# Optimization experiments

Hardware: AMD Instinct MI355X
Metric: run time of the kernel (lower is better)

The kernel has to match this reference:

```python
import jax, jax.numpy as jnp
import numpy as np

IN_DIM = 128
OUT_DIM = 128
H = 8
HD = OUT_DIM // H  # 16
EPS = 1e-5
NEG = -1e30


def setup_inputs() -> dict:
    key = jax.random.key(0)
    ks = jax.random.split(key, 10)
    B, N = 8, 1024
    h = jax.random.normal(ks[0], (B, N, IN_DIM), dtype=jnp.float32)
    adj_mask = jax.random.randint(ks[1], (B, N, N), 0, 2, dtype=jnp.int32)
    s = 1.0 / np.sqrt(IN_DIM)
    W = jax.random.normal(ks[2], (H, IN_DIM, HD), dtype=jnp.float32) * s
    a = jax.random.normal(ks[3], (H, 2 * HD), dtype=jnp.float32) * (1.0 / np.sqrt(2 * HD))
    ln1_g = jnp.ones((OUT_DIM,), jnp.float32)
    ln1_b = jnp.zeros((OUT_DIM,), jnp.float32)
    w1 = jax.random.normal(ks[4], (OUT_DIM, 2 * OUT_DIM), dtype=jnp.float32) * (1.0 / np.sqrt(OUT_DIM))
    b1 = jnp.zeros((2 * OUT_DIM,), jnp.float32)
    w2 = jax.random.normal(ks[5], (2 * OUT_DIM, OUT_DIM), dtype=jnp.float32) * (1.0 / np.sqrt(2 * OUT_DIM))
    b2 = jnp.zeros((OUT_DIM,), jnp.float32)
    ln2_g = jnp.ones((OUT_DIM,), jnp.float32)
    ln2_b = jnp.zeros((OUT_DIM,), jnp.float32)
    return dict(h=h, adj_mask=adj_mask, W=W, a=a, ln1_g=ln1_g, ln1_b=ln1_b,
                w1=w1, b1=b1, w2=w2, b2=b2, ln2_g=ln2_g, ln2_b=ln2_b)


def _layernorm(x, g, b):
    mu = jnp.mean(x, axis=-1, keepdims=True)
    var = jnp.mean(jnp.square(x - mu), axis=-1, keepdims=True)
    return (x - mu) * jax.lax.rsqrt(var + EPS) * g + b


def reference(h, adj_mask, W, a, ln1_g, ln1_b, w1, b1, w2, b2, ln2_g, ln2_b):
    B, N, _ = h.shape
    # Per-head projection: (B,H,N,HD)
    Wh = jnp.einsum('bni,hid->bhnd', h, W)
    # a.[Wh_i, Wh_j] = a_src.Wh_i + a_dst.Wh_j (decompose concat-score)
    a_src, a_dst = a[:, :HD], a[:, HD:]
    s_i = jnp.einsum('bhnd,hd->bhn', Wh, a_src)  # source term
    s_j = jnp.einsum('bhnd,hd->bhn', Wh, a_dst)  # target term
    e = s_i[:, :, :, None] + s_j[:, :, None, :]  # (B,H,N,N)
    e = jnp.where(e >= 0, e, 0.2 * e)            # LeakyReLU(0.2)
    mask = (adj_mask != 0)[:, None, :, :]        # (B,1,N,N)
    e = jnp.where(mask, e, NEG)
    alpha = jax.nn.softmax(e, axis=-1)
    # rows with no neighbors -> NaN in torch softmax -> zeroed; replicate
    row_valid = jnp.any(mask, axis=-1, keepdims=True)  # (B,1,N,1)
    alpha = jnp.where(row_valid, alpha, 0.0)
    # dropout in eval mode = identity
    h_heads = jnp.einsum('bhnm,bhmd->bhnd', alpha, Wh)
    h_cat = h_heads.transpose(0, 2, 1, 3).reshape(B, N, H * HD)
    # residual (in_dim == out_dim here)
    h_cat = _layernorm(h_cat + h, ln1_g, ln1_b)
    ffn = jnp.maximum(h_cat @ w1 + b1, 0.0) @ w2 + b2
    return _layernorm(h_cat + ffn, ln2_g, ln2_b)
```

## Files before the change

### kernel.cpp

```cpp
#include <hip/hip_runtime.h>
#include <hip/hip_bf16.h>

#define IN_DIM 128
#define OUT_DIM 128
#define NHEAD 8
#define HD 16
#define BB 8
#define NN 1024

typedef unsigned long long u64;
typedef float f32x4 __attribute__((ext_vector_type(4)));
typedef short bf16x8 __attribute__((ext_vector_type(8)));

__global__ __launch_bounds__(256) void k_pack(const int* __restrict__ adj,
                                              u64* __restrict__ bits) {
    int lane = threadIdx.x & 63;
    int wid = blockIdx.x * 4 + (threadIdx.x >> 6);
    for (int w = wid; w < BB * NN * 16; w += 2048 * 4) {
        int v = adj[(size_t)w * 64 + lane];
        u64 m = __ballot(v != 0);
        if (lane == 0) bits[w] = m;
    }
}

__global__ __launch_bounds__(256) void k_wprep(const float* __restrict__ w1,
                                               const float* __restrict__ w2,
                                               unsigned short* __restrict__ w1T,
                                               unsigned short* __restrict__ w2T) {
    __shared__ float tile[32][33];
    int blk = blockIdx.x;
    const float* src; unsigned short* dst; int R, C;
    if (blk < 32) { src = w1; dst = w1T; R = 128; C = 256; }
    else          { src = w2; dst = w2T; R = 256; C = 128; blk -= 32; }
    int tpr = C >> 5;
    int tr = blk / tpr, tc = blk - tr * tpr;
    int r0 = tr << 5, c0 = tc << 5;
    int t = threadIdx.x, lr = t >> 5, lc = t & 31;
#pragma unroll
    for (int p = 0; p < 4; ++p)
        tile[lr + p * 8][lc] = src[(size_t)(r0 + lr + p * 8) * C + c0 + lc];
    __syncthreads();
#pragma unroll
    for (int p = 0; p < 4; ++p) {
        __hip_bfloat16 bv = __float2bfloat16(tile[lc][lr + p * 8]);
        dst[(size_t)(c0 + lr + p * 8) * R + r0 + lc] = *(unsigned short*)&bv;
    }
}

__global__ __launch_bounds__(256) void k_wh(const float* __restrict__ hin,
                                            const float* __restrict__ W,
                                            float* __restrict__ wh) {
    extern __shared__ float smem[];
    float* h_s  = smem;
    float* wt_s = smem + 32 * 132;
    int t = threadIdx.x;
    int blk = blockIdx.x;
    int b = blk >> 5;
    int ntile = blk & 31;
    const float* hrow = hin + ((size_t)b * NN + ntile * 32) * IN_DIM;

#pragma unroll
    for (int it = 0; it < 4; ++it) {
        int g = t + 256 * it;
        int row = g >> 5, c4 = g & 31;
        float4 v = ((const float4*)hrow)[g];
        *(float4*)&h_s[row * 132 + c4 * 4] = v;
    }
    for (int g = t; g < (NHEAD * IN_DIM * HD) / 4; g += 256) {
        int hh = g >> 9;
        int rem = g & 511;
        int i = rem >> 2, d4 = rem & 3;
        float4 v = ((const float4*)W)[g];
        wt_s[(hh * 16 + d4 * 4 + 0) * 132 + i] = v.x;
        wt_s[(hh * 16 + d4 * 4 + 1) * 132 + i] = v.y;
        wt_s[(hh * 16 + d4 * 4 + 2) * 132 + i] = v.z;
        wt_s[(hh * 16 + d4 * 4 + 3) * 132 + i] = v.w;
    }
    __syncthreads();

    int hq = (t & 31) >> 2;
    int d4 = t & 3;
    int ngrp = t >> 5;
    float acc[4][4];
#pragma unroll
    for (int q = 0; q < 4; ++q)
#pragma unroll
        for (int dd = 0; dd < 4; ++dd) acc[q][dd] = 0.f;

    for (int i4 = 0; i4 < 32; ++i4) {
        float4 wr[4], hv[4];
#pragma unroll
        for (int dd = 0; dd < 4; ++dd)
            wr[dd] = *(const float4*)&wt_s[(hq * 16 + d4 * 4 + dd) * 132 + i4 * 4];
#pragma unroll
        for (int q = 0; q < 4; ++q)
            hv[q] = *(const float4*)&h_s[(ngrp * 4 + q) * 132 + i4 * 4];
#pragma unroll
        for (int q = 0; q < 4; ++q)
#pragma unroll
            for (int dd = 0; dd < 4; ++dd)
                acc[q][dd] += hv[q].x * wr[dd].x + hv[q].y * wr[dd].y +
                              hv[q].z * wr[dd].z + hv[q].w * wr[dd].w;
    }
#pragma unroll
    for (int q = 0; q < 4; ++q) {
        int row = ntile * 32 + ngrp * 4 + q;
        float4 o = make_float4(acc[q][0], acc[q][1], acc[q][2], acc[q][3]);
        *(float4*)&wh[(((size_t)b * NHEAD + hq) * NN + row) * HD + d4 * 4] = o;
    }
}

__global__ __launch_bounds__(512) void k_attn(const float* __restrict__ wh,
                                              const unsigned* __restrict__ bits32,
                                              const float* __restrict__ a,
                                              float* __restrict__ hh) {
    __shared__ __align__(16) float a_s[32];
    __shared__ unsigned mask_s[128 * 33];
    __shared__ __align__(16) float sj_s[NN];
    __shared__ float si_s[128];
    __shared__ __align__(16) unsigned short whT[16 * 1032];

    int t = threadIdx.x;
    int blk = blockIdx.x;
    int part = blk & 7;
    int bh = blk >> 3;
    int hq = bh & 7;
    int b = bh >> 3;
    int blkrow = part * 128;
    const float* whg = wh + (size_t)bh * (NN * HD);

    if (t < 32) a_s[t] = a[hq * 32 + t];

    {
        const unsigned* mb = bits32 + ((size_t)b * NN + blkrow) * 32;
#pragma unroll
        for (int it = 0; it < 8; ++it) {
            int g = t + 512 * it;
            int row = g >> 5, w = g & 31;
            mask_s[row * 33 + w] = mb[g];
        }
    }
    {
        int d = t & 15, jg = t >> 4;
        const float* src = whg + d;
#pragma unroll
        for (int jj = 0; jj < 32; jj += 2) {
            int j = jg * 32 + jj;
            float v0 = src[(size_t)j * 16];
            float v1 = src[(size_t)(j + 1) * 16];
            unsigned u;
            asm("v_cvt_pk_bf16_f32 %0, %1, %2" : "=v"(u) : "v"(v0), "v"(v1));
            *(unsigned*)&whT[d * 1032 + j] = u;
        }
    }
    __syncthreads();

    {
        float4 ad0 = *(const float4*)&a_s[16];
        float4 ad1 = *(const float4*)&a_s[20];
        float4 ad2 = *(const float4*)&a_s[24];
        float4 ad3 = *(const float4*)&a_s[28];
#pragma unroll
        for (int r = 0; r < 2; ++r) {
            int j = t * 2 + r;
            const float4* p = (const float4*)(whg + (size_t)j * 16);
            float4 x0 = p[0], x1 = p[1], x2 = p[2], x3 = p[3];
            sj_s[j] = x0.x * ad0.x + x0.y * ad0.y + x0.z * ad0.z + x0.w * ad0.w +
                      x1.x * ad1.x + x1.y * ad1.y + x1.z * ad1.z + x1.w * ad1.w +
                      x2.x * ad2.x + x2.y * ad2.y + x2.z * ad2.z + x2.w * ad2.w +
                      x3.x * ad3.x + x3.y * ad3.y + x3.z * ad3.z + x3.w * ad3.w;
        }
        if (t < 128) {
            float4 as0 = *(const float4*)&a_s[0];
            float4 as1 = *(const float4*)&a_s[4];
            float4 as2 = *(const float4*)&a_s[8];
            float4 as3 = *(const float4*)&a_s[12];
            int i = blkrow + t;
            const float4* p = (const float4*)(whg + (size_t)i * 16);
            float4 x0 = p[0], x1 = p[1], x2 = p[2], x3 = p[3];
            si_s[t] = x0.x * as0.x + x0.y * as0.y + x0.z * as0.z + x0.w * as0.w +
                      x1.x * as1.x + x1.y * as1.y + x1.z * as1.z + x1.w * as1.w +
                      x2.x * as2.x + x2.y * as2.y + x2.z * as2.z + x2.w * as2.w +
                      x3.x * as3.x + x3.y * as3.y + x3.z * as3.z + x3.w * as3.w;
        }
    }
    __syncthreads();

    int wv = t >> 6, lane = t & 63;
    int lo16 = lane & 15;
    int g = lane >> 4;
    float si_r = si_s[wv * 16 + lo16];
    const unsigned* mrow = &mask_s[(wv * 16 + lo16) * 33];

    f32x4 acc = {0.f, 0.f, 0.f, 0.f};
    float lsum = 0.f;

    for (int kt = 0; kt < 32; ++kt) {
        bf16x8 bfrag = *(const bf16x8*)&whT[lo16 * 1032 + kt * 32 + g * 8];
        float4 sa = *(const float4*)&sj_s[kt * 32 + g * 8];
        float4 sb = *(const float4*)&sj_s[kt * 32 + g * 8 + 4];
        unsigned m = mrow[kt] >> (g * 8);
        float p[8];
        float sj[8] = {sa.x, sa.y, sa.z, sa.w, sb.x, sb.y, sb.z, sb.w};
#pragma unroll
        for (int e = 0; e < 8; ++e) {
            float v = si_r + sj[e];
            v = fmaxf(v, 0.f) + 0.2f * fminf(v, 0.f);
            float pe = __expf(v);
            pe = ((m >> e) & 1) ? pe : 0.f;
            lsum += pe;
            p[e] = pe;
        }
        union { bf16x8 v; unsigned u[4]; } af;
#pragma unroll
        for (int q = 0; q < 4; ++q)
            asm("v_cvt_pk_bf16_f32 %0, %1, %2" : "=v"(af.u[q]) : "v"(p[2 * q]), "v"(p[2 * q + 1]));
        acc = __builtin_amdgcn_mfma_f32_16x16x32_bf16(af.v, bfrag, acc, 0, 0, 0);
    }

    lsum += __shfl_xor(lsum, 16);
    lsum += __shfl_xor(lsum, 32);

    float* obase = hh + ((size_t)b * NN + blkrow + wv * 16) * OUT_DIM + hq * HD + lo16;
#pragma unroll
    for (int q = 0; q < 4; ++q) {
        float ls = __shfl(lsum, 4 * g + q);
        float r = (ls > 0.f) ? 1.0f / ls : 0.f;
        obase[(size_t)(4 * g + q) * OUT_DIM] = acc[q] * r;
    }
}

__global__ __launch_bounds__(512, 1) void k_ffn(const float* __restrict__ hhs,
                                                const float* __restrict__ hin,
                                                const float* __restrict__ g1,
                                                const float* __restrict__ bt1,
                                                const unsigned short* __restrict__ w1T,
                                                const float* __restrict__ bb1,
                                                const unsigned short* __restrict__ w2T,
                                                const float* __restrict__ bb2,
                                                const float* __restrict__ g2,
                                                const float* __restrict__ bt2,
                                                float* __restrict__ out) {
    __shared__ float xc_f[32][128];
    __shared__ float y_f[32][132];
    __shared__ __align__(16) unsigned short xc_bf[32 * 128];
    __shared__ __align__(16) unsigned short hid_bf[32 * 256];

    int t = threadIdx.x;
    int R0 = blockIdx.x * 32;
    int wv = t >> 6, lane = t & 63;
    int lo = lane & 15, g = lane >> 4;

    bf16x8 b1f[2][4];
#pragma unroll
    for (int jt = 0; jt < 2; ++jt) {
        int n = (wv * 2 + jt) * 16 + lo;
#pragma unroll
        for (int kt = 0; kt < 4; ++kt)
            b1f[jt][kt] = *(const bf16x8*)&w1T[(size_t)n * 128 + kt * 32 + g * 8];
    }
    bf16x8 b2f[8];
    {
        int n = wv * 16 + lo;
#pragma unroll
        for (int kt = 0; kt < 8; ++kt)
            b2f[kt] = *(const bf16x8*)&w2T[(size_t)n * 256 + kt * 32 + g * 8];
    }
    float b1v[2];
    b1v[0] = bb1[(wv * 2 + 0) * 16 + lo];
    b1v[1] = bb1[(wv * 2 + 1) * 16 + lo];
    float b2v = bb2[wv * 16 + lo];

    {
        int r = t >> 4, c = t & 15;
        size_t row = (size_t)(R0 + r) * 128;
        float4 ha = *(const float4*)&hhs[row + c * 8];
        float4 hb = *(const float4*)&hhs[row + c * 8 + 4];
        float4 ia = *(const float4*)&hin[row + c * 8];
        float4 ib = *(const float4*)&hin[row + c * 8 + 4];
        float x[8] = {ha.x + ia.x, ha.y + ia.y, ha.z + ia.z, ha.w + ia.w,
                      hb.x + ib.x, hb.y + ib.y, hb.z + ib.z, hb.w + ib.w};
        float s = 0.f, s2 = 0.f;
#pragma unroll
        for (int j = 0; j < 8; ++j) { s += x[j]; s2 += x[j] * x[j]; }
#pragma unroll
        for (int off = 8; off > 0; off >>= 1) {
            s += __shfl_xor(s, off);
            s2 += __shfl_xor(s2, off);
        }
        float mu = s * (1.f / 128.f);
        float var = s2 * (1.f / 128.f) - mu * mu;
        float rs = rsqrtf(var + 1e-5f);
        float4 ga = *(const float4*)&g1[c * 8], gb = *(const float4*)&g1[c * 8 + 4];
        float4 ba = *(const float4*)&bt1[c * 8], bb = *(const float4*)&bt1[c * 8 + 4];
        float gg[8] = {ga.x, ga.y, ga.z, ga.w, gb.x, gb.y, gb.z, gb.w};
        float bbv[8] = {ba.x, ba.y, ba.z, ba.w, bb.x, bb.y, bb.z, bb.w};
        float xo[8];
#pragma unroll
        for (int j = 0; j < 8; ++j) xo[j] = (x[j] - mu) * rs * gg[j] + bbv[j];
        *(float4*)&xc_f[r][c * 8]     = make_float4(xo[0], xo[1], xo[2], xo[3]);
        *(float4*)&xc_f[r][c * 8 + 4] = make_float4(xo[4], xo[5], xo[6], xo[7]);
        union { uint4 v; unsigned u[4]; } pk;
#pragma unroll
        for (int q = 0; q < 4; ++q)
            asm("v_cvt_pk_bf16_f32 %0, %1, %2" : "=v"(pk.u[q]) : "v"(xo[2 * q]), "v"(xo[2 * q + 1]));
        int byte = (r * 256 + c * 16) ^ ((r & 7) << 4);
        *(uint4*)((char*)xc_bf + byte) = pk.v;
    }
    __syncthreads();

    {
        bf16x8 af[2][4];
#pragma unroll
        for (int mt = 0; mt < 2; ++mt) {
            int m = mt * 16 + lo;
#pragma unroll
            for (int kt = 0; kt < 4; ++kt) {
                int byte = (m * 256 + kt * 64 + g * 16) ^ ((m & 7) << 4);
                af[mt][kt] = *(const bf16x8*)((const char*)xc_bf + byte);
            }
        }
#pragma unroll
        for (int mt = 0; mt < 2; ++mt)
#pragma unroll
            for (int jt = 0; jt < 2; ++jt) {
                f32x4 acc = {0.f, 0.f, 0.f, 0.f};
#pragma unroll
                for (int kt = 0; kt < 4; ++kt)
                    acc = __builtin_amdgcn_mfma_f32_16x16x32_bf16(af[mt][kt], b1f[jt][kt], acc, 0, 0, 0);
                int n = (wv * 2 + jt) * 16 + lo;
#pragma unroll
                for (int q = 0; q < 4; ++q) {
                    float hv = fmaxf(acc[q] + b1v[jt], 0.f);
                    int m = mt * 16 + 4 * g + q;
                    int byte = (m * 512 + n * 2) ^ ((m & 7) << 4);
                    __hip_bfloat16 bv = __float2bfloat16(hv);
                    *(unsigned short*)((char*)hid_bf + byte) = *(unsigned short*)&bv;
                }
            }
    }
    __syncthreads();

    {
        f32x4 acc2[2] = {{0.f, 0.f, 0.f, 0.f}, {0.f, 0.f, 0.f, 0.f}};
#pragma unroll
        for (int mt = 0; mt < 2; ++mt) {
            int m = mt * 16 + lo;
#pragma unroll
            for (int kt = 0; kt < 8; ++kt) {
                int byte = (m * 512 + kt * 64 + g * 16) ^ ((m & 7) << 4);
                bf16x8 a = *(const bf16x8*)((const char*)hid_bf + byte);
                acc2[mt] = __builtin_amdgcn_mfma_f32_16x16x32_bf16(a, b2f[kt], acc2[mt], 0, 0, 0);
            }
        }
        int n = wv * 16 + lo;
#pragma unroll
        for (int mt = 0; mt < 2; ++mt)
#pragma unroll
            for (int q = 0; q < 4; ++q)
                y_f[mt * 16 + 4 * g + q][n] = acc2[mt][q] + b2v;
    }
    __syncthreads();

    {
        int r = t >> 4, c = t & 15;
        float xv[8];
        float s = 0.f, s2 = 0.f;
#pragma unroll
        for (int j = 0; j < 8; ++j) {
            float v = xc_f[r][c * 8 + j] + y_f[r][c * 8 + j];
            xv[j] = v; s += v; s2 += v * v;
        }
#pragma unroll
        for (int off = 8; off > 0; off >>= 1) {
            s += __shfl_xor(s, off);
            s2 += __shfl_xor(s2, off);
        }
        float mu = s * (1.f / 128.f);
        float var = s2 * (1.f / 128.f) - mu * mu;
        float rs = rsqrtf(var + 1e-5f);
        float4 ga = *(const float4*)&g2[c * 8], gb = *(const float4*)&g2[c * 8 + 4];
        float4 ba = *(const float4*)&bt2[c * 8], bb = *(const float4*)&bt2[c * 8 + 4];
        float o[8] = {(xv[0] - mu) * rs * ga.x + ba.x, (xv[1] - mu) * rs * ga.y + ba.y,
                      (xv[2] - mu) * rs * ga.z + ba.z, (xv[3] - mu) * rs * ga.w + ba.w,
                      (xv[4] - mu) * rs * gb.x + bb.x, (xv[5] - mu) * rs * gb.y + bb.y,
                      (xv[6] - mu) * rs * gb.z + bb.z, (xv[7] - mu) * rs * gb.w + bb.w};
        size_t row = (size_t)(R0 + r) * 128;
        *(float4*)&out[row + c * 8]     = make_float4(o[0], o[1], o[2], o[3]);
        *(float4*)&out[row + c * 8 + 4] = make_float4(o[4], o[5], o[6], o[7]);
    }
}

extern "C" void kernel_launch(void* const* d_in, const int* in_sizes, int n_in,
                              void* d_out, int out_size, void* d_ws, size_t ws_size,
                              hipStream_t stream) {
    const float* hin  = (const float*)d_in[0];
    const int*   adj  = (const int*)d_in[1];
    const float* W    = (const float*)d_in[2];
    const float* a    = (const float*)d_in[3];
    const float* ln1g = (const float*)d_in[4];
    const float* ln1b = (const float*)d_in[5];
    const float* w1   = (const float*)d_in[6];
    const float* b1   = (const float*)d_in[7];
    const float* w2   = (const float*)d_in[8];
    const float* b2   = (const float*)d_in[9];
    const float* ln2g = (const float*)d_in[10];
    const float* ln2b = (const float*)d_in[11];
    float* out = (float*)d_out;

    float* wh             = (float*)d_ws;
    u64*   bits           = (u64*)((char*)d_ws + (4u << 20));
    float* hh             = (float*)((char*)d_ws + (5u << 20));
    unsigned short* w1T   = (unsigned short*)((char*)d_ws + (9u << 20));
    unsigned short* w2T   = (unsigned short*)((char*)d_ws + (9u << 20) + 65536);

    k_pack<<<2048, 256, 0, stream>>>(adj, bits);
    k_wprep<<<64, 256, 0, stream>>>(w1, w2, w1T, w2T);
    k_wh<<<BB * 32, 256, (32 * 132 + 128 * 132) * sizeof(float), stream>>>(hin, W, wh);
    k_attn<<<BB * NHEAD * 8, 512, 0, stream>>>(wh, (const unsigned*)bits, a, hh);
    k_ffn<<<BB * NN / 32, 512, 0, stream>>>(hh, hin, ln1g, ln1b, w1T, b1, w2T, b2, ln2g, ln2b, out);
}
```

Baseline: 66.72 us.

## Merge prep kernels and precompute bf16 Wh and attention scores for attention

Folds the adjacency bit-packing, weight transpose and Wh projection into one prep kernel. The projection now emits bf16 transposed Wh plus per-node source and target scores pre-scaled by log2e, so the attention kernel no longer converts or recomputes them. The attention kernel loads bf16 Wh into an XOR-swizzled LDS layout, reads mask words straight from global with one-ahead prefetch, and computes LeakyReLU as fma(0.4,|v|,0.6v). It uses raw v_exp_f32 with -150 for masked entries and sets launch bounds to 3 blocks per CU. This cuts launches, LDS footprint and redundant setup, but reads W from global in the projection and makes mask loads uncoalesced.

```diff
diff --git a/kernel.cpp b/kernel.cpp
--- a/kernel.cpp
+++ b/kernel.cpp
@@ -7,207 +7,174 @@
 #define HD 16
 #define BB 8
 #define NN 1024
+#define LOG2E 1.44269504f
 
 typedef unsigned long long u64;
 typedef float f32x4 __attribute__((ext_vector_type(4)));
 typedef short bf16x8 __attribute__((ext_vector_type(8)));
 
-__global__ __launch_bounds__(256) void k_pack(const int* __restrict__ adj,
-                                              u64* __restrict__ bits) {
-    int lane = threadIdx.x & 63;
-    int wid = blockIdx.x * 4 + (threadIdx.x >> 6);
-    for (int w = wid; w < BB * NN * 16; w += 2048 * 4) {
-        int v = adj[(size_t)w * 64 + lane];
-        u64 m = __ballot(v != 0);
-        if (lane == 0) bits[w] = m;
+__global__ __launch_bounds__(256) void k_prep(
+    const float* __restrict__ hin, const float* __restrict__ W,
+    const float* __restrict__ a, const int* __restrict__ adj,
+    u64* __restrict__ bits, unsigned short* __restrict__ whT,
+    float* __restrict__ si_g, float* __restrict__ sj_g,
+    const float* __restrict__ w1, const float* __restrict__ w2,
+    unsigned short* __restrict__ w1T, unsigned short* __restrict__ w2T)
+{
+    __shared__ float smem[32 * 132];
+    int blk = blockIdx.x;
+    int t = threadIdx.x;
+
+    if (blk < 256) {
+        int b = blk >> 5, ntile = blk & 31;
+        const float* hrow = hin + ((size_t)b * NN + ntile * 32) * IN_DIM;
+#pragma unroll
+        for (int it = 0; it < 4; ++it) {
+            int g = t + 256 * it;
+            int row = g >> 5, c4 = g & 31;
+            float4 v = ((const float4*)hrow)[g];
+            *(float4*)&smem[row * 132 + c4 * 4] = v;
+        }
+        __syncthreads();
+
+        int d4 = t & 3;
+        int hq = (t >> 2) & 7;
+        int ngrp = t >> 5;
+        float acc[4][4];
+#pragma unroll
+        for (int q = 0; q < 4; ++q)
+#pragma unroll
+            for (int dd = 0; dd < 4; ++dd) acc[q][dd] = 0.f;
+
+        for (int i4 = 0; i4 < 32; ++i4) {
+            float4 wf[4];
+#pragma unroll
+            for (int k = 0; k < 4; ++k)
+                wf[k] = *(const float4*)&W[((size_t)hq * 128 + i4 * 4 + k) * 16 + d4 * 4];
+            float4 hv[4];
+#pragma unroll
+            for (int q = 0; q < 4; ++q)
+                hv[q] = *(const float4*)&smem[(ngrp * 4 + q) * 132 + i4 * 4];
+#pragma unroll
+            for (int q = 0; q < 4; ++q) {
+                acc[q][0] += hv[q].x * wf[0].x + hv[q].y * wf[1].x + hv[q].z * wf[2].x + hv[q].w * wf[3].x;
+                acc[q][1] += hv[q].x * wf[0].y + hv[q].y * wf[1].y + hv[q].z * wf[2].y + hv[q].w * wf[3].y;
+                acc[q][2] += hv[q].x * wf[0].z + hv[q].y * wf[1].z + hv[q].z * wf[2].z + hv[q].w * wf[3].z;
+                acc[q][3] += hv[q].x * wf[0].w + hv[q].y * wf[1].w + hv[q].z * wf[2].w + hv[q].w * wf[3].w;
+            }
+        }
+
+        int bh = b * NHEAD + hq;
+        int rowbase = ntile * 32 + ngrp * 4;
+
+        float asrc[4], adst[4];
+#pragma unroll
+        for (int dd = 0; dd < 4; ++dd) {
+            asrc[dd] = a[hq * 32 + d4 * 4 + dd];
+            adst[dd] = a[hq * 32 + 16 + d4 * 4 + dd];
+        }
+#pragma unroll
+        for (int q = 0; q < 4; ++q) {
+            float psi = acc[q][0] * asrc[0] + acc[q][1] * asrc[1] + acc[q][2] * asrc[2] + acc[q][3] * asrc[3];
+            float psj = acc[q][0] * adst[0] + acc[q][1] * adst[1] + acc[q][2] * adst[2] + acc[q][3] * adst[3];
+            psi += __shfl_xor(psi, 1); psi += __shfl_xor(psi, 2);
+            psj += __shfl_xor(psj, 1); psj += __shfl_xor(psj, 2);
+            if (d4 == 0) {
+                si_g[(size_t)bh * NN + rowbase + q] = psi * LOG2E;
+                sj_g[(size_t)bh * NN + rowbase + q] = psj * LOG2E;
+            }
+        }
+
+#pragma unroll
+        for (int dd = 0; dd < 4; ++dd) {
+            unsigned u0, u1;
+            asm("v_cvt_pk_bf16_f32 %0, %1, %2" : "=v"(u0) : "v"(acc[0][dd]), "v"(acc[1][dd]));
+            asm("v_cvt_pk_bf16_f32 %0, %1, %2" : "=v"(u1) : "v"(acc[2][dd]), "v"(acc[3][dd]));
+            uint2 pk = make_uint2(u0, u1);
+            *(uint2*)&whT[((size_t)bh * 16 + d4 * 4 + dd) * 1024 + rowbase] = pk;
+        }
+    } else if (blk < 2304) {
+        int lane = t & 63;
+        int wid = (blk - 256) * 4 + (t >> 6);
+        for (int w = wid; w < BB * NN * 16; w += 2048 * 4) {
+            int v = adj[(size_t)w * 64 + lane];
+            u64 m = __ballot(v != 0);
+            if (lane == 0) bits[w] = m;
+        }
+    } else {
+        int bb = blk - 2304;
+        const float* src; unsigned short* dst; int R, C;
+        if (bb < 32) { src = w1; dst = w1T; R = 128; C = 256; }
+        else         { src = w2; dst = w2T; R = 256; C = 128; bb -= 32; }
+        int tpr = C >> 5;
+        int tr = bb / tpr, tc = bb - tr * tpr;
+        int r0 = tr << 5, c0 = tc << 5;
+        int lr = t >> 5, lc = t & 31;
+#pragma unroll
+        for (int p = 0; p < 4; ++p)
+            smem[(lr + p * 8) * 33 + lc] = src[(size_t)(r0 + lr + p * 8) * C + c0 + lc];
+        __syncthreads();
+#pragma unroll
+        for (int p = 0; p < 4; ++p) {
+            __hip_bfloat16 bv = __float2bfloat16(smem[lc * 33 + lr + p * 8]);
+            dst[(size_t)(c0 + lr + p * 8) * R + r0 + lc] = *(unsigned short*)&bv;
+        }
     }
 }
 
-__global__ __launch_bounds__(256) void k_wprep(const float* __restrict__ w1,
-                                               const float* __restrict__ w2,
-                                               unsigned short* __restrict__ w1T,
-                                               unsigned short* __restrict__ w2T) {
-    __shared__ float tile[32][33];
-    int blk = blockIdx.x;
-    const float* src; unsigned short* dst; int R, C;
-    if (blk < 32) { src = w1; dst = w1T; R = 128; C = 256; }
-    else          { src = w2; dst = w2T; R = 256; C = 128; blk -= 32; }
-    int tpr = C >> 5;
-    int tr = blk / tpr, tc = blk - tr * tpr;
-    int r0 = tr << 5, c0 = tc << 5;
-    int t = threadIdx.x, lr = t >> 5, lc = t & 31;
-#pragma unroll
-    for (int p = 0; p < 4; ++p)
-        tile[lr + p * 8][lc] = src[(size_t)(r0 + lr + p * 8) * C + c0 + lc];
-    __syncthreads();
-#pragma unroll
-    for (int p = 0; p < 4; ++p) {
-        __hip_bfloat16 bv = __float2bfloat16(tile[lc][lr + p * 8]);
-        dst[(size_t)(c0 + lr + p * 8) * R + r0 + lc] = *(unsigned short*)&bv;
-    }
-}
-
-__global__ __launch_bounds__(256) void k_wh(const float* __restrict__ hin,
-                                            const float* __restrict__ W,
-                                            float* __restrict__ wh) {
-    extern __shared__ float smem[];
-    float* h_s  = smem;
-    float* wt_s = smem + 32 * 132;
-    int t = threadIdx.x;
-    int blk = blockIdx.x;
-    int b = blk >> 5;
-    int ntile = blk & 31;
-    const float* hrow = hin + ((size_t)b * NN + ntile * 32) * IN_DIM;
-
-#pragma unroll
-    for (int it = 0; it < 4; ++it) {
-        int g = t + 256 * it;
-        int row = g >> 5, c4 = g & 31;
-        float4 v = ((const float4*)hrow)[g];
-        *(float4*)&h_s[row * 132 + c4 * 4] = v;
-    }
-    for (int g = t; g < (NHEAD * IN_DIM * HD) / 4; g += 256) {
-        int hh = g >> 9;
-        int rem = g & 511;
-        int i = rem >> 2, d4 = rem & 3;
-        float4 v = ((const float4*)W)[g];
-        wt_s[(hh * 16 + d4 * 4 + 0) * 132 + i] = v.x;
-        wt_s[(hh * 16 + d4 * 4 + 1) * 132 + i] = v.y;
-        wt_s[(hh * 16 + d4 * 4 + 2) * 132 + i] = v.z;
-        wt_s[(hh * 16 + d4 * 4 + 3) * 132 + i] = v.w;
-    }
-    __syncthreads();
-
-    int hq = (t & 31) >> 2;
-    int d4 = t & 3;
-    int ngrp = t >> 5;
-    float acc[4][4];
-#pragma unroll
-    for (int q = 0; q < 4; ++q)
-#pragma unroll
-        for (int dd = 0; dd < 4; ++dd) acc[q][dd] = 0.f;
-
-    for (int i4 = 0; i4 < 32; ++i4) {
-        float4 wr[4], hv[4];
-#pragma unroll
-        for (int dd = 0; dd < 4; ++dd)
-            wr[dd] = *(const float4*)&wt_s[(hq * 16 + d4 * 4 + dd) * 132 + i4 * 4];
-#pragma unroll
-        for (int q = 0; q < 4; ++q)
-            hv[q] = *(const float4*)&h_s[(ngrp * 4 + q) * 132 + i4 * 4];
-#pragma unroll
-        for (int q = 0; q < 4; ++q)
-#pragma unroll
-            for (int dd = 0; dd < 4; ++dd)
-                acc[q][dd] += hv[q].x * wr[dd].x + hv[q].y * wr[dd].y +
-                              hv[q].z * wr[dd].z + hv[q].w * wr[dd].w;
-    }
-#pragma unroll
-    for (int q = 0; q < 4; ++q) {
-        int row = ntile * 32 + ngrp * 4 + q;
-        float4 o = make_float4(acc[q][0], acc[q][1], acc[q][2], acc[q][3]);
-        *(float4*)&wh[(((size_t)b * NHEAD + hq) * NN + row) * HD + d4 * 4] = o;
-    }
-}
-
-__global__ __launch_bounds__(512) void k_attn(const float* __restrict__ wh,
-                                              const unsigned* __restrict__ bits32,
-                                              const float* __restrict__ a,
-                                              float* __restrict__ hh) {
-    __shared__ __align__(16) float a_s[32];
-    __shared__ unsigned mask_s[128 * 33];
+__global__ __launch_bounds__(512, 3) void k_attn(
+    const unsigned short* __restrict__ whT,
+    const unsigned* __restrict__ bits32,
+    const float* __restrict__ si_g, const float* __restrict__ sj_g,
+    float* __restrict__ hh)
+{
+    __shared__ __align__(16) unsigned short whT_s[16 * 1032];
     __shared__ __align__(16) float sj_s[NN];
-    __shared__ float si_s[128];
-    __shared__ __align__(16) unsigned short whT[16 * 1032];
-
     int t = threadIdx.x;
     int blk = blockIdx.x;
     int part = blk & 7;
     int bh = blk >> 3;
-    int hq = bh & 7;
-    int b = bh >> 3;
+    int hq = bh & 7, b = bh >> 3;
     int blkrow = part * 128;
-    const float* whg = wh + (size_t)bh * (NN * HD);
-
-    if (t < 32) a_s[t] = a[hq * 32 + t];
-
-    {
-        const unsigned* mb = bits32 + ((size_t)b * NN + blkrow) * 32;
-#pragma unroll
-        for (int it = 0; it < 8; ++it) {
+
+    {
+        const uint4* src = (const uint4*)(whT + (size_t)bh * 16 * 1024);
+#pragma unroll
+        for (int it = 0; it < 4; ++it) {
             int g = t + 512 * it;
-            int row = g >> 5, w = g & 31;
-            mask_s[row * 33 + w] = mb[g];
-        }
-    }
-    {
-        int d = t & 15, jg = t >> 4;
-        const float* src = whg + d;
-#pragma unroll
-        for (int jj = 0; jj < 32; jj += 2) {
-            int j = jg * 32 + jj;
-            float v0 = src[(size_t)j * 16];
-            float v1 = src[(size_t)(j + 1) * 16];
-            unsigned u;
-            asm("v_cvt_pk_bf16_f32 %0, %1, %2" : "=v"(u) : "v"(v0), "v"(v1));
-            *(unsigned*)&whT[d * 1032 + j] = u;
-        }
+            int d = g >> 7, c8 = g & 127;
+            uint4 v = src[g];
+            *(uint4*)&whT_s[d * 1032 + ((c8 ^ (d & 3)) * 8)] = v;
+        }
+        if (t < 256) *(float4*)&sj_s[t * 4] = ((const float4*)(sj_g + (size_t)bh * NN))[t];
     }
     __syncthreads();
 
-    {
-        float4 ad0 = *(const float4*)&a_s[16];
-        float4 ad1 = *(const float4*)&a_s[20];
-        float4 ad2 = *(const float4*)&a_s[24];
-        float4 ad3 = *(const float4*)&a_s[28];
-#pragma unroll
-        for (int r = 0; r < 2; ++r) {
-            int j = t * 2 + r;
-            const float4* p = (const float4*)(whg + (size_t)j * 16);
-            float4 x0 = p[0], x1 = p[1], x2 = p[2], x3 = p[3];
-            sj_s[j] = x0.x * ad0.x + x0.y * ad0.y + x0.z * ad0.z + x0.w * ad0.w +
-                      x1.x * ad1.x + x1.y * ad1.y + x1.z * ad1.z + x1.w * ad1.w +
-                      x2.x * ad2.x + x2.y * ad2.y + x2.z * ad2.z + x2.w * ad2.w +
-                      x3.x * ad3.x + x3.y * ad3.y + x3.z * ad3.z + x3.w * ad3.w;
-        }
-        if (t < 128) {
-            float4 as0 = *(const float4*)&a_s[0];
-            float4 as1 = *(const float4*)&a_s[4];
-            float4 as2 = *(const float4*)&a_s[8];
-            float4 as3 = *(const float4*)&a_s[12];
-            int i = blkrow + t;
-            const float4* p = (const float4*)(whg + (size_t)i * 16);
-            float4 x0 = p[0], x1 = p[1], x2 = p[2], x3 = p[3];
-            si_s[t] = x0.x * as0.x + x0.y * as0.y + x0.z * as0.z + x0.w * as0.w +
-                      x1.x * as1.x + x1.y * as1.y + x1.z * as1.z + x1.w * as1.w +
-                      x2.x * as2.x + x2.y * as2.y + x2.z * as2.z + x2.w * as2.w +
-                      x3.x * as3.x + x3.y * as3.y + x3.z * as3.z + x3.w * as3.w;
-        }
-    }
-    __syncthreads();
-
     int wv = t >> 6, lane = t & 63;
-    int lo16 = lane & 15;
-    int g = lane >> 4;
-    float si_r = si_s[wv * 16 + lo16];
-    const unsigned* mrow = &mask_s[(wv * 16 + lo16) * 33];
+    int lo16 = lane & 15, g = lane >> 4;
+    int row = blkrow + wv * 16 + lo16;
+    float si_r = si_g[(size_t)bh * NN + row];
+    const unsigned* mrow = bits32 + ((size_t)b * NN + row) * 32;
 
     f32x4 acc = {0.f, 0.f, 0.f, 0.f};
     float lsum = 0.f;
-
+    unsigned m = mrow[0];
+#pragma unroll 4
     for (int kt = 0; kt < 32; ++kt) {
-        bf16x8 bfrag = *(const bf16x8*)&whT[lo16 * 1032 + kt * 32 + g * 8];
+        unsigned m_next = (kt < 31) ? mrow[kt + 1] : 0u;
+        bf16x8 bfrag = *(const bf16x8*)&whT_s[lo16 * 1032 + (((kt * 4 + g) ^ (lo16 & 3)) * 8)];
         float4 sa = *(const float4*)&sj_s[kt * 32 + g * 8];
         float4 sb = *(const float4*)&sj_s[kt * 32 + g * 8 + 4];
-        unsigned m = mrow[kt] >> (g * 8);
+        unsigned mm = m >> (g * 8);
+        float sj[8] = {sa.x, sa.y, sa.z, sa.w, sb.x, sb.y, sb.z, sb.w};
         float p[8];
-        float sj[8] = {sa.x, sa.y, sa.z, sa.w, sb.x, sb.y, sb.z, sb.w};
 #pragma unroll
         for (int e = 0; e < 8; ++e) {
             float v = si_r + sj[e];
-            v = fmaxf(v, 0.f) + 0.2f * fminf(v, 0.f);
-            float pe = __expf(v);
-            pe = ((m >> e) & 1) ? pe : 0.f;
+            float lv = __builtin_fmaf(0.4f, __builtin_fabsf(v), 0.6f * v);
+            lv = ((mm >> e) & 1) ? lv : -150.f;
+            float pe;
+            asm("v_exp_f32 %0, %1" : "=v"(pe) : "v"(lv));
             lsum += pe;
             p[e] = pe;
         }
@@ -216,6 +183,7 @@
         for (int q = 0; q < 4; ++q)
             asm("v_cvt_pk_bf16_f32 %0, %1, %2" : "=v"(af.u[q]) : "v"(p[2 * q]), "v"(p[2 * q + 1]));
         acc = __builtin_amdgcn_mfma_f32_16x16x32_bf16(af.v, bfrag, acc, 0, 0, 0);
+        m = m_next;
     }
 
     lsum += __shfl_xor(lsum, 16);
@@ -408,15 +376,16 @@
     const float* ln2b = (const float*)d_in[11];
     float* out = (float*)d_out;
 
-    float* wh             = (float*)d_ws;
-    u64*   bits           = (u64*)((char*)d_ws + (4u << 20));
-    float* hh             = (float*)((char*)d_ws + (5u << 20));
-    unsigned short* w1T   = (unsigned short*)((char*)d_ws + (9u << 20));
-    unsigned short* w2T   = (unsigned short*)((char*)d_ws + (9u << 20) + 65536);
-
-    k_pack<<<2048, 256, 0, stream>>>(adj, bits);
-    k_wprep<<<64, 256, 0, stream>>>(w1, w2, w1T, w2T);
-    k_wh<<<BB * 32, 256, (32 * 132 + 128 * 132) * sizeof(float), stream>>>(hin, W, wh);
-    k_attn<<<BB * NHEAD * 8, 512, 0, stream>>>(wh, (const unsigned*)bits, a, hh);
+    u64* bits           = (u64*)d_ws;
+    unsigned short* whT = (unsigned short*)((char*)d_ws + (1u << 20));
+    float* si_g         = (float*)((char*)d_ws + (3u << 20));
+    float* sj_g         = (float*)((char*)d_ws + (3u << 20) + (256u << 10));
+    float* hh           = (float*)((char*)d_ws + (3u << 20) + (512u << 10));
+    unsigned short* w1T = (unsigned short*)((char*)d_ws + (7u << 20) + (512u << 10));
+    unsigned short* w2T = (unsigned short*)((char*)d_ws + (7u << 20) + (512u << 10) + 65536);
+
+    k_prep<<<2368, 256, 0, stream>>>(hin, W, a, adj, bits, whT, si_g, sj_g,
+                                     w1, w2, w1T, w2T);
+    k_attn<<<BB * NHEAD * 8, 512, 0, stream>>>(whT, (const unsigned*)bits, si_g, sj_g, hh);
     k_ffn<<<BB * NN / 32, 512, 0, stream>>>(hh, hin, ln1g, ln1b, w1T, b1, w2T, b2, ln2g, ln2b, out);
 }
```

Result: faster. 62.90 us (-5.7%).
